# Kernel optimization log

Measured on AMD Instinct MI355X. Metric: run time of the kernel, lower is better.

The kernel has to match this reference:

```python
import jax, jax.numpy as jnp
import numpy as np

DIM = 512
NUM_HEADS = 16
HEAD_DIM = DIM // NUM_HEADS
HIDDEN = int(DIM * 4.0)
EPS = 1e-5


def layer_norm(x, gamma, beta):
    mu = jnp.mean(x, axis=-1, keepdims=True)
    var = jnp.mean(jnp.square(x - mu), axis=-1, keepdims=True)
    return (x - mu) * jax.lax.rsqrt(var + EPS) * gamma + beta


def setup_inputs() -> dict:
    key = jax.random.key(0)
    ks = jax.random.split(key, 8)
    B, L, C = 32, 3136, DIM
    x = jax.random.normal(ks[0], (B, L, C), dtype=jnp.float32)
    norm1_g = jnp.ones((C,), jnp.float32)
    norm1_b = jnp.zeros((C,), jnp.float32)
    # spatial (per-head) mixing weight: (num_heads, head_dim, head_dim)
    w_spatial = jax.random.normal(ks[1], (NUM_HEADS, HEAD_DIM, HEAD_DIM), jnp.float32) * (1.0 / np.sqrt(HEAD_DIM))
    norm2_g = jnp.ones((C,), jnp.float32)
    norm2_b = jnp.zeros((C,), jnp.float32)
    w1 = jax.random.normal(ks[2], (C, HIDDEN), jnp.float32) * (1.0 / np.sqrt(C))
    b1 = jnp.zeros((HIDDEN,), jnp.float32)
    w2 = jax.random.normal(ks[3], (HIDDEN, C), jnp.float32) * (1.0 / np.sqrt(HIDDEN))
    b2 = jnp.zeros((C,), jnp.float32)
    return {"x": x, "norm1_g": norm1_g, "norm1_b": norm1_b, "w_spatial": w_spatial,
            "norm2_g": norm2_g, "norm2_b": norm2_b, "w1": w1, "b1": b1, "w2": w2, "b2": b2}


def reference(x, norm1_g, norm1_b, w_spatial, norm2_g, norm2_b, w1, b1, w2, b2):
    B, L, C = x.shape
    shortcut = x
    h = layer_norm(x, norm1_g, norm1_b)
    # window partition -> per-head channel-sub-dim linear (shared across windows/positions)
    # mathematically equivalent to applying the per-head matmul at every token
    h = h.reshape(B, L, NUM_HEADS, HEAD_DIM)
    h = jnp.einsum('blhd,hde->blhe', h, w_spatial)
    h = h.reshape(B, L, C)
    x = shortcut + h
    # channel MLP: Linear -> GELU(tanh) -> Linear
    y = layer_norm(x, norm2_g, norm2_b)
    y = jax.nn.gelu(y @ w1 + b1, approximate=True)
    y = y @ w2 + b2
    return x + y
```

## Files before the change

kernel.cpp:

```cpp
#include <hip/hip_runtime.h>
#include <hip/hip_bf16.h>


typedef __bf16 bf16x8 __attribute__((ext_vector_type(8)));
typedef float f32x4 __attribute__((ext_vector_type(4)));

constexpr int CDIM = 512;
constexpr int HID = 2048;
constexpr int MROWS = 32 * 3136;
constexpr float LN_EPS = 1e-5f;

static __device__ __forceinline__ float gelu_tanh(float x) {
  const float u = 0.7978845608028654f * fmaf(0.044715f * x * x, x, x);
  const float e = __expf(2.0f * u);
  return 0.5f * x * (2.0f - 2.0f / (e + 1.0f));
}

static __device__ __forceinline__ void load_lds16(const void* g, void* l) {
  __builtin_amdgcn_global_load_lds((__attribute__((address_space(1))) void*)g,
                                   (__attribute__((address_space(3))) void*)l,
                                   16, 0, 0);
}

template <int KD, int ND>
__global__ __launch_bounds__(256) void cvt_t(const float* __restrict__ src,
                                             __hip_bfloat16* __restrict__ dst) {
  __shared__ float tl[64][65];
  const int t = threadIdx.x;
  constexpr int NTN = ND / 64;
  const int k0 = (blockIdx.x / NTN) * 64;
  const int n0 = (blockIdx.x % NTN) * 64;
  const int c4 = (t & 15) * 4;
  const int r = t >> 4;
#pragma unroll
  for (int j = 0; j < 4; ++j) {
    const int kk = r + j * 16;
    const float4 v = *(const float4*)&src[(size_t)(k0 + kk) * ND + n0 + c4];
    tl[c4 + 0][kk] = v.x;
    tl[c4 + 1][kk] = v.y;
    tl[c4 + 2][kk] = v.z;
    tl[c4 + 3][kk] = v.w;
  }
  __syncthreads();
#pragma unroll
  for (int j = 0; j < 4; ++j) {
    const int nn = r + j * 16;
    __hip_bfloat16 o[4];
#pragma unroll
    for (int c = 0; c < 4; ++c) o[c] = __float2bfloat16(tl[nn][c4 + c]);
    *(uint2*)&dst[(size_t)(n0 + nn) * KD + k0 + c4] = *(const uint2*)o;
  }
}

__global__ __launch_bounds__(256) void fused_pre(
    const float* __restrict__ x, const float* __restrict__ g1,
    const float* __restrict__ b1, const float* __restrict__ wsp,
    const float* __restrict__ g2, const float* __restrict__ b2,
    float* __restrict__ x2out, __hip_bfloat16* __restrict__ yout) {
  __shared__ float lnbuf[2][CDIM];
  __shared__ float red[16];

  const int t = threadIdx.x;
  const int lane = t & 63;
  const int w = t >> 6;
  const int c0 = 2 * t;
  const int hd = c0 >> 5, e0 = c0 & 31;

  float wc0[32], wc1[32];
#pragma unroll
  for (int d = 0; d < 32; ++d) {
    const float2 wv = *(const float2*)&wsp[(hd * 32 + d) * 32 + e0];
    wc0[d] = wv.x;
    wc1[d] = wv.y;
  }
  const float2 g1v = *(const float2*)&g1[c0];
  const float2 b1v = *(const float2*)&b1[c0];
  const float2 g2v = *(const float2*)&g2[c0];
  const float2 b2v = *(const float2*)&b2[c0];

  for (int rp = blockIdx.x; rp < MROWS / 2; rp += gridDim.x) {
    const size_t ra = (size_t)rp * 2, rb = ra + 1;
    const float2 xa = *(const float2*)&x[ra * CDIM + c0];
    const float2 xb = *(const float2*)&x[rb * CDIM + c0];

    float sa = xa.x + xa.y, qa = xa.x * xa.x + xa.y * xa.y;
    float sb = xb.x + xb.y, qb = xb.x * xb.x + xb.y * xb.y;
#pragma unroll
    for (int off = 32; off; off >>= 1) {
      sa += __shfl_down(sa, off);
      qa += __shfl_down(qa, off);
      sb += __shfl_down(sb, off);
      qb += __shfl_down(qb, off);
    }
    if (lane == 0) {
      red[w * 4 + 0] = sa;
      red[w * 4 + 1] = qa;
      red[w * 4 + 2] = sb;
      red[w * 4 + 3] = qb;
    }
    __syncthreads();
    sa = red[0] + red[4] + red[8] + red[12];
    qa = red[1] + red[5] + red[9] + red[13];
    sb = red[2] + red[6] + red[10] + red[14];
    qb = red[3] + red[7] + red[11] + red[15];
    float mua = sa * (1.0f / CDIM), mub = sb * (1.0f / CDIM);
    float rsa = rsqrtf(qa * (1.0f / CDIM) - mua * mua + LN_EPS);
    float rsb = rsqrtf(qb * (1.0f / CDIM) - mub * mub + LN_EPS);
    lnbuf[0][c0] = (xa.x - mua) * rsa * g1v.x + b1v.x;
    lnbuf[0][c0 + 1] = (xa.y - mua) * rsa * g1v.y + b1v.y;
    lnbuf[1][c0] = (xb.x - mub) * rsb * g1v.x + b1v.x;
    lnbuf[1][c0 + 1] = (xb.y - mub) * rsb * g1v.y + b1v.y;
    __syncthreads();

    float ha0 = 0.f, ha1 = 0.f, hb0 = 0.f, hb1 = 0.f;
#pragma unroll
    for (int d = 0; d < 32; ++d) {
      const float la = lnbuf[0][hd * 32 + d];
      const float lb = lnbuf[1][hd * 32 + d];
      ha0 = fmaf(la, wc0[d], ha0);
      ha1 = fmaf(la, wc1[d], ha1);
      hb0 = fmaf(lb, wc0[d], hb0);
      hb1 = fmaf(lb, wc1[d], hb1);
    }
    const float a0 = xa.x + ha0, a1 = xa.y + ha1;
    const float b0 = xb.x + hb0, b1r = xb.y + hb1;
    float2 av;
    av.x = a0;
    av.y = a1;
    *(float2*)&x2out[ra * CDIM + c0] = av;
    av.x = b0;
    av.y = b1r;
    *(float2*)&x2out[rb * CDIM + c0] = av;

    sa = a0 + a1;
    qa = a0 * a0 + a1 * a1;
    sb = b0 + b1r;
    qb = b0 * b0 + b1r * b1r;
#pragma unroll
    for (int off = 32; off; off >>= 1) {
      sa += __shfl_down(sa, off);
      qa += __shfl_down(qa, off);
      sb += __shfl_down(sb, off);
      qb += __shfl_down(qb, off);
    }
    if (lane == 0) {
      red[w * 4 + 0] = sa;
      red[w * 4 + 1] = qa;
      red[w * 4 + 2] = sb;
      red[w * 4 + 3] = qb;
    }
    __syncthreads();
    sa = red[0] + red[4] + red[8] + red[12];
    qa = red[1] + red[5] + red[9] + red[13];
    sb = red[2] + red[6] + red[10] + red[14];
    qb = red[3] + red[7] + red[11] + red[15];
    mua = sa * (1.0f / CDIM);
    mub = sb * (1.0f / CDIM);
    rsa = rsqrtf(qa * (1.0f / CDIM) - mua * mua + LN_EPS);
    rsb = rsqrtf(qb * (1.0f / CDIM) - mub * mub + LN_EPS);
    __hip_bfloat162 yv;
    yv.x = __float2bfloat16((a0 - mua) * rsa * g2v.x + b2v.x);
    yv.y = __float2bfloat16((a1 - mua) * rsa * g2v.y + b2v.y);
    *(__hip_bfloat162*)&yout[ra * CDIM + c0] = yv;
    yv.x = __float2bfloat16((b0 - mub) * rsb * g2v.x + b2v.x);
    yv.y = __float2bfloat16((b1r - mub) * rsb * g2v.y + b2v.y);
    *(__hip_bfloat162*)&yout[rb * CDIM + c0] = yv;
    __syncthreads();
  }
}

template <int N, bool GELU>
static __device__ __forceinline__ void epilogue(const f32x4 (&acc)[8][4],
                                                char* smb, int tid, int lane,
                                                int wm, int wn, size_t am0,
                                                int bn0,
                                                const float* __restrict__ bias,
                                                __hip_bfloat16* __restrict__ zout,
                                                float* __restrict__ fout) {
  const int cr = (lane >> 4) * 4;
  const int cc = lane & 15;
  if constexpr (GELU) {
    __syncthreads();
    __hip_bfloat16* ot = (__hip_bfloat16*)smb;
#pragma unroll
    for (int n = 0; n < 4; ++n) {
      const int col = wn * 64 + n * 16 + cc;
      const float bv = bias[bn0 + col];
#pragma unroll
      for (int m = 0; m < 8; ++m) {
        const int row = wm * 128 + m * 16 + cr;
#pragma unroll
        for (int j = 0; j < 4; ++j)
          ot[(row + j) * 256 + col] =
              __float2bfloat16(gelu_tanh(acc[m][n][j] + bv));
      }
    }
    __syncthreads();
#pragma unroll
    for (int it = 0; it < 16; ++it) {
      const int seg = it * 512 + tid;
      const int row = seg >> 5, cs = seg & 31;
      const uint4 v = *(const uint4*)(smb + seg * 16);
      *(uint4*)&zout[(am0 + row) * N + bn0 + cs * 8] = v;
    }
  } else {
    float* ot = (float*)smb;
#pragma unroll
    for (int p = 0; p < 2; ++p) {
      __syncthreads();
      if (wm == p) {
#pragma unroll
        for (int n = 0; n < 4; ++n) {
          const int col = wn * 64 + n * 16 + cc;
          const float bv = bias[bn0 + col];
#pragma unroll
          for (int m = 0; m < 8; ++m) {
            const int rl = m * 16 + cr;
#pragma unroll
            for (int j = 0; j < 4; ++j)
              ot[(rl + j) * 256 + col] = acc[m][n][j] + bv;
          }
        }
      }
      __syncthreads();
#pragma unroll
      for (int it = 0; it < 16; ++it) {
        const int seg = it * 512 + tid;
        const int row = seg >> 6, cs = seg & 63;
        const float4 lv = *(const float4*)(smb + seg * 16);
        float* gp = &fout[(am0 + p * 128 + row) * N + bn0 + cs * 4];
        float4 o = *(const float4*)gp;
        o.x += lv.x;
        o.y += lv.y;
        o.z += lv.z;
        o.w += lv.w;
        *(float4*)gp = o;
      }
    }
  }
}

template <int K, int N, bool GELU>
__global__ __launch_bounds__(512) void gemmpp(
    const __hip_bfloat16* __restrict__ A, const __hip_bfloat16* __restrict__ Bt,
    const float* __restrict__ bias, __hip_bfloat16* __restrict__ zout,
    float* __restrict__ fout) {
  constexpr int NT = N / 256;
  constexpr int NKT = K / 32;
  __shared__ __attribute__((aligned(16))) __hip_bfloat16 lds[4][2][256 * 32];

  const int tid = threadIdx.x;
  const int lane = tid & 63;
  const int w = tid >> 6;
  const int wm = w >> 2, wn = w & 3;

  const int cpx = gridDim.x >> 3;
  const int bid = (blockIdx.x & 7) * cpx + (blockIdx.x >> 3);
  const int tm = bid / NT, tn = bid - tm * NT;
  const size_t am0 = (size_t)tm * 256;
  const int bn0 = tn * 256;

  const int r0 = tid >> 2;
  const int q0 = tid & 3;
  const __hip_bfloat16* aP0 = A + (am0 + r0) * K + q0 * 8;
  const __hip_bfloat16* aP1 = aP0 + (size_t)128 * K;
  const __hip_bfloat16* bP0 = Bt + (size_t)(bn0 + r0) * K + q0 * 8;
  const __hip_bfloat16* bP1 = bP0 + (size_t)128 * K;
  const int lo0 = (w * 64) * 8;
  const int lo1 = (512 + w * 64) * 8;

#define STAGE_A(sl, kt)                            \
  do {                                             \
    load_lds16(aP0 + (kt) * 32, &lds[sl][0][lo0]); \
    load_lds16(aP1 + (kt) * 32, &lds[sl][0][lo1]); \
  } while (0)
#define STAGE_B(sl, kt)                            \
  do {                                             \
    load_lds16(bP0 + (kt) * 32, &lds[sl][1][lo0]); \
    load_lds16(bP1 + (kt) * 32, &lds[sl][1][lo1]); \
  } while (0)

  const int fr = lane & 15;
  const int kb = (lane >> 4) * 16;

#define LD_A03(sl)                                                          \
  do {                                                                      \
    _Pragma("unroll") for (int m = 0; m < 4; ++m) a03[m] =                  \
        *(const bf16x8*)((const char*)&lds[sl][0][0] +                      \
                         (wm * 128 + m * 16 + fr) * 64 + kb);               \
  } while (0)
#define LD_A47(sl)                                                          \
  do {                                                                      \
    _Pragma("unroll") for (int m = 0; m < 4; ++m) a47[m] =                  \
        *(const bf16x8*)((const char*)&lds[sl][0][0] +                      \
                         (wm * 128 + (m + 4) * 16 + fr) * 64 + kb);         \
  } while (0)
#define LD_B(sl)                                                            \
  do {                                                                      \
    _Pragma("unroll") for (int n = 0; n < 4; ++n) bf[n] =                   \
        *(const bf16x8*)((const char*)&lds[sl][1][0] +                      \
                         (wn * 64 + n * 16 + fr) * 64 + kb);                \
  } while (0)

  f32x4 acc[8][4] = {};
  bf16x8 a03[4], a47[4], bf[4];

  STAGE_A(0, 0);
  STAGE_B(0, 0);
  STAGE_A(1, 1);
  STAGE_B(1, 1);
  asm volatile("s_waitcnt vmcnt(4)" ::: "memory");
  __builtin_amdgcn_s_barrier();
  LD_A03(0);
  LD_B(0);

  for (int t = 0; t < NKT; ++t) {
    const int sl = t & 3, sl1 = (t + 1) & 3, sl2 = (t + 2) & 3;
    const bool pf2 = (t + 2) < NKT, pf1 = (t + 1) < NKT;

    if (pf2) STAGE_A(sl2, t + 2);
    __builtin_amdgcn_s_setprio(1);
#pragma unroll
    for (int m = 0; m < 4; ++m)
#pragma unroll
      for (int n = 0; n < 4; ++n)
        acc[m][n] = __builtin_amdgcn_mfma_f32_16x16x32_bf16(a03[m], bf[n],
                                                            acc[m][n], 0, 0, 0);
    __builtin_amdgcn_s_setprio(0);
    LD_A47(sl);

    if (pf2)
      asm volatile("s_waitcnt vmcnt(2)" ::: "memory");
    else
      asm volatile("s_waitcnt vmcnt(0)" ::: "memory");
    __builtin_amdgcn_s_barrier();

    if (pf2) STAGE_B(sl2, t + 2);
    __builtin_amdgcn_s_setprio(1);
#pragma unroll
    for (int m = 0; m < 4; ++m)
#pragma unroll
      for (int n = 0; n < 4; ++n)
        acc[m + 4][n] = __builtin_amdgcn_mfma_f32_16x16x32_bf16(
            a47[m], bf[n], acc[m + 4][n], 0, 0, 0);
    __builtin_amdgcn_s_setprio(0);
    if (pf1) {
      LD_A03(sl1);
      LD_B(sl1);
    }
    __builtin_amdgcn_s_barrier();
  }
#undef STAGE_A
#undef STAGE_B
#undef LD_A03
#undef LD_A47
#undef LD_B

  epilogue<N, GELU>(acc, (char*)&lds[0][0][0], tid, lane, wm, wn, am0, bn0,
                    bias, zout, fout);
}

extern "C" void kernel_launch(void* const* d_in, const int* in_sizes, int n_in,
                              void* d_out, int out_size, void* d_ws,
                              size_t ws_size, hipStream_t stream) {
  const float* x = (const float*)d_in[0];
  const float* n1g = (const float*)d_in[1];
  const float* n1b = (const float*)d_in[2];
  const float* wsp = (const float*)d_in[3];
  const float* n2g = (const float*)d_in[4];
  const float* n2b = (const float*)d_in[5];
  const float* w1 = (const float*)d_in[6];
  const float* b1 = (const float*)d_in[7];
  const float* w2 = (const float*)d_in[8];
  const float* b2 = (const float*)d_in[9];
  float* out = (float*)d_out;

  __hip_bfloat16* ybuf = (__hip_bfloat16*)d_ws;
  __hip_bfloat16* zbuf = ybuf + (size_t)MROWS * CDIM;
  __hip_bfloat16* w1t = zbuf + (size_t)MROWS * HID;
  __hip_bfloat16* w2t = w1t + (size_t)CDIM * HID;

  cvt_t<CDIM, HID><<<(CDIM / 64) * (HID / 64), 256, 0, stream>>>(w1, w1t);
  cvt_t<HID, CDIM><<<(HID / 64) * (CDIM / 64), 256, 0, stream>>>(w2, w2t);
  fused_pre<<<2048, 256, 0, stream>>>(x, n1g, n1b, wsp, n2g, n2b, out, ybuf);
  gemmpp<CDIM, HID, true><<<(MROWS / 256) * (HID / 256), 512, 0, stream>>>(
      ybuf, w1t, b1, zbuf, nullptr);
  gemmpp<HID, CDIM, false><<<(MROWS / 256) * (CDIM / 256), 512, 0, stream>>>(
      zbuf, w2t, b2, nullptr, out);
}
```

Measured before the change: 921.7 us.

## Load GEMM fragments directly from global memory instead of staging through LDS

Replaces the LDS-staged, double-barriered pipeline in the bf16 MFMA GEMMs with direct per-wave global loads of A and B fragments into registers every k-step. This drops the barriers and the LDS round trip. In exchange it loses cross-wave data sharing, so global/L2 traffic rises several-fold and the loads go out as uncoalesced 16-byte strided reads, with no explicit prefetch beyond loop unrolling. The LDS array is kept only as scratch for the epilogue.

```diff
diff --git a/kernel.cpp b/kernel.cpp
--- a/kernel.cpp
+++ b/kernel.cpp
@@ -14,12 +14,6 @@
   const float u = 0.7978845608028654f * fmaf(0.044715f * x * x, x, x);
   const float e = __expf(2.0f * u);
   return 0.5f * x * (2.0f - 2.0f / (e + 1.0f));
-}
-
-static __device__ __forceinline__ void load_lds16(const void* g, void* l) {
-  __builtin_amdgcn_global_load_lds((__attribute__((address_space(1))) void*)g,
-                                   (__attribute__((address_space(3))) void*)l,
-                                   16, 0, 0);
 }
 
 template <int KD, int ND>
@@ -241,13 +235,13 @@
 }
 
 template <int K, int N, bool GELU>
-__global__ __launch_bounds__(512) void gemmpp(
+__global__ __launch_bounds__(512) void gemmdr(
     const __hip_bfloat16* __restrict__ A, const __hip_bfloat16* __restrict__ Bt,
     const float* __restrict__ bias, __hip_bfloat16* __restrict__ zout,
     float* __restrict__ fout) {
   constexpr int NT = N / 256;
   constexpr int NKT = K / 32;
-  __shared__ __attribute__((aligned(16))) __hip_bfloat16 lds[4][2][256 * 32];
+  __shared__ __attribute__((aligned(16))) __hip_bfloat16 lds[256 * 256];
 
   const int tid = threadIdx.x;
   const int lane = tid & 63;
@@ -260,104 +254,34 @@
   const size_t am0 = (size_t)tm * 256;
   const int bn0 = tn * 256;
 
-  const int r0 = tid >> 2;
-  const int q0 = tid & 3;
-  const __hip_bfloat16* aP0 = A + (am0 + r0) * K + q0 * 8;
-  const __hip_bfloat16* aP1 = aP0 + (size_t)128 * K;
-  const __hip_bfloat16* bP0 = Bt + (size_t)(bn0 + r0) * K + q0 * 8;
-  const __hip_bfloat16* bP1 = bP0 + (size_t)128 * K;
-  const int lo0 = (w * 64) * 8;
-  const int lo1 = (512 + w * 64) * 8;
-
-#define STAGE_A(sl, kt)                            \
-  do {                                             \
-    load_lds16(aP0 + (kt) * 32, &lds[sl][0][lo0]); \
-    load_lds16(aP1 + (kt) * 32, &lds[sl][0][lo1]); \
-  } while (0)
-#define STAGE_B(sl, kt)                            \
-  do {                                             \
-    load_lds16(bP0 + (kt) * 32, &lds[sl][1][lo0]); \
-    load_lds16(bP1 + (kt) * 32, &lds[sl][1][lo1]); \
-  } while (0)
-
   const int fr = lane & 15;
-  const int kb = (lane >> 4) * 16;
-
-#define LD_A03(sl)                                                          \
-  do {                                                                      \
-    _Pragma("unroll") for (int m = 0; m < 4; ++m) a03[m] =                  \
-        *(const bf16x8*)((const char*)&lds[sl][0][0] +                      \
-                         (wm * 128 + m * 16 + fr) * 64 + kb);               \
-  } while (0)
-#define LD_A47(sl)                                                          \
-  do {                                                                      \
-    _Pragma("unroll") for (int m = 0; m < 4; ++m) a47[m] =                  \
-        *(const bf16x8*)((const char*)&lds[sl][0][0] +                      \
-                         (wm * 128 + (m + 4) * 16 + fr) * 64 + kb);         \
-  } while (0)
-#define LD_B(sl)                                                            \
-  do {                                                                      \
-    _Pragma("unroll") for (int n = 0; n < 4; ++n) bf[n] =                   \
-        *(const bf16x8*)((const char*)&lds[sl][1][0] +                      \
-                         (wn * 64 + n * 16 + fr) * 64 + kb);                \
-  } while (0)
+  const int kg = lane >> 4;
+
+  const __hip_bfloat16* aR = A + (am0 + wm * 128 + fr) * K + kg * 8;
+  const __hip_bfloat16* bR = Bt + (size_t)(bn0 + wn * 64 + fr) * K + kg * 8;
 
   f32x4 acc[8][4] = {};
-  bf16x8 a03[4], a47[4], bf[4];
-
-  STAGE_A(0, 0);
-  STAGE_B(0, 0);
-  STAGE_A(1, 1);
-  STAGE_B(1, 1);
-  asm volatile("s_waitcnt vmcnt(4)" ::: "memory");
-  __builtin_amdgcn_s_barrier();
-  LD_A03(0);
-  LD_B(0);
-
+
+#pragma unroll 4
   for (int t = 0; t < NKT; ++t) {
-    const int sl = t & 3, sl1 = (t + 1) & 3, sl2 = (t + 2) & 3;
-    const bool pf2 = (t + 2) < NKT, pf1 = (t + 1) < NKT;
-
-    if (pf2) STAGE_A(sl2, t + 2);
-    __builtin_amdgcn_s_setprio(1);
-#pragma unroll
-    for (int m = 0; m < 4; ++m)
+    const int kof = t * 32;
+    bf16x8 af[8], bf[4];
+#pragma unroll
+    for (int m = 0; m < 8; ++m)
+      af[m] = *(const bf16x8*)(aR + (size_t)(m * 16) * K + kof);
+#pragma unroll
+    for (int n = 0; n < 4; ++n)
+      bf[n] = *(const bf16x8*)(bR + (size_t)(n * 16) * K + kof);
+#pragma unroll
+    for (int m = 0; m < 8; ++m)
 #pragma unroll
       for (int n = 0; n < 4; ++n)
-        acc[m][n] = __builtin_amdgcn_mfma_f32_16x16x32_bf16(a03[m], bf[n],
+        acc[m][n] = __builtin_amdgcn_mfma_f32_16x16x32_bf16(af[m], bf[n],
                                                             acc[m][n], 0, 0, 0);
-    __builtin_amdgcn_s_setprio(0);
-    LD_A47(sl);
-
-    if (pf2)
-      asm volatile("s_waitcnt vmcnt(2)" ::: "memory");
-    else
-      asm volatile("s_waitcnt vmcnt(0)" ::: "memory");
-    __builtin_amdgcn_s_barrier();
-
-    if (pf2) STAGE_B(sl2, t + 2);
-    __builtin_amdgcn_s_setprio(1);
-#pragma unroll
-    for (int m = 0; m < 4; ++m)
-#pragma unroll
-      for (int n = 0; n < 4; ++n)
-        acc[m + 4][n] = __builtin_amdgcn_mfma_f32_16x16x32_bf16(
-            a47[m], bf[n], acc[m + 4][n], 0, 0, 0);
-    __builtin_amdgcn_s_setprio(0);
-    if (pf1) {
-      LD_A03(sl1);
-      LD_B(sl1);
-    }
-    __builtin_amdgcn_s_barrier();
-  }
-#undef STAGE_A
-#undef STAGE_B
-#undef LD_A03
-#undef LD_A47
-#undef LD_B
-
-  epilogue<N, GELU>(acc, (char*)&lds[0][0][0], tid, lane, wm, wn, am0, bn0,
-                    bias, zout, fout);
+  }
+
+  epilogue<N, GELU>(acc, (char*)lds, tid, lane, wm, wn, am0, bn0, bias, zout,
+                    fout);
 }
 
 extern "C" void kernel_launch(void* const* d_in, const int* in_sizes, int n_in,
@@ -383,8 +307,8 @@
   cvt_t<CDIM, HID><<<(CDIM / 64) * (HID / 64), 256, 0, stream>>>(w1, w1t);
   cvt_t<HID, CDIM><<<(HID / 64) * (CDIM / 64), 256, 0, stream>>>(w2, w2t);
   fused_pre<<<2048, 256, 0, stream>>>(x, n1g, n1b, wsp, n2g, n2b, out, ybuf);
-  gemmpp<CDIM, HID, true><<<(MROWS / 256) * (HID / 256), 512, 0, stream>>>(
+  gemmdr<CDIM, HID, true><<<(MROWS / 256) * (HID / 256), 512, 0, stream>>>(
       ybuf, w1t, b1, zbuf, nullptr);
-  gemmpp<HID, CDIM, false><<<(MROWS / 256) * (CDIM / 256), 512, 0, stream>>>(
+  gemmdr<HID, CDIM, false><<<(MROWS / 256) * (CDIM / 256), 512, 0, stream>>>(
       zbuf, w2t, b2, nullptr, out);
 }
```

Result: slower. 1.848 ms (+100.5%).
